# Kernel optimization log

Hardware: AMD Instinct MI355X
Metric: run time of the kernel (lower is better)

The kernel has to match this reference:

```python
import jax, jax.numpy as jnp
import numpy as np

NUM_BITS = 10
MEM_SIZE = 2 ** NUM_BITS  # 1024
HIDDEN = 1024
INPUT = 1024
BATCH = 16384
LN_EPS = 1e-5


def setup_inputs() -> dict:
    key = jax.random.key(0)
    ks = jax.random.split(key, 8)
    s = 0.02
    return {
        "x": jax.random.normal(ks[0], (BATCH, INPUT), jnp.float32),
        "h_prev": jax.random.normal(ks[1], (BATCH, HIDDEN), jnp.float32),
        "memory": jax.random.normal(ks[2], (MEM_SIZE, HIDDEN), jnp.float32),
        "W_w": jax.random.normal(ks[3], (HIDDEN, INPUT), jnp.float32) * s,
        "W_b": jnp.zeros((HIDDEN,), jnp.float32),
        "U_w": jax.random.normal(ks[4], (HIDDEN, HIDDEN), jnp.float32) * s,
        "U_b": jnp.zeros((HIDDEN,), jnp.float32),
        "Q_w": jax.random.normal(ks[5], (HIDDEN, HIDDEN), jnp.float32) * s,
        "Q_b": jnp.zeros((HIDDEN,), jnp.float32),
        "M_w": jax.random.normal(ks[6], (NUM_BITS, HIDDEN), jnp.float32) * s,
        "M_b": jnp.zeros((NUM_BITS,), jnp.float32),
        "ln_g": jnp.ones((HIDDEN,), jnp.float32),
        "ln_b": jnp.zeros((HIDDEN,), jnp.float32),
    }


def reference(x, h_prev, memory, W_w, W_b, U_w, U_b, Q_w, Q_b, M_w, M_b, ln_g, ln_b):
    # Binary address from h_prev (eval-mode hard threshold, non-differentiable)
    powers = jnp.asarray(2 ** np.arange(NUM_BITS - 1, -1, -1), dtype=x.dtype)  # [num_bits]
    logits = h_prev @ M_w.T + M_b                              # [B, num_bits]
    binary = (jax.nn.sigmoid(logits) > 0.5).astype(x.dtype)    # hard bits
    index = jnp.clip((binary * powers).sum(-1).astype(jnp.int32), 0, MEM_SIZE - 1)  # [B]
    h_mem = memory[index]                                      # gather [B, H]
    # Fused linear combine + LayerNorm + sigmoid
    pre = x @ W_w.T + W_b + h_prev @ U_w.T + U_b + h_mem @ Q_w.T + Q_b  # [B, H]
    mu = pre.mean(-1, keepdims=True)
    var = ((pre - mu) ** 2).mean(-1, keepdims=True)            # biased var (torch LN)
    norm = (pre - mu) * jax.lax.rsqrt(var + LN_EPS)
    return jax.nn.sigmoid(norm * ln_g + ln_b)                  # h_new [B, H]
```

## Files before the change

kernel.cpp:

```cpp
#include <hip/hip_runtime.h>

#define BATCH   16384
#define HIDDEN  1024
#define K2      2048
#define MEMSZ   1024
#define NBITS   10

#define BM 256
#define BN 256
#define BK 64
#define NT (K2 / BK)

#define MQB     64
#define U_BM    262144
#define U_TOT   2359296
#define SBLK    2304
#define SSTRIDE (SBLK * 256)
#define BBLK    (BATCH / 8)

typedef __bf16 bf16x8 __attribute__((ext_vector_type(8)));
typedef float  f32x4  __attribute__((ext_vector_type(4)));
typedef unsigned short u16x8 __attribute__((ext_vector_type(8)));

__device__ __forceinline__ unsigned short f2bf(float f) {
    unsigned int u = __float_as_uint(f);
    u += 0x7FFFu + ((u >> 16) & 1u);
    return (unsigned short)(u >> 16);
}

__device__ __forceinline__ u16x8 f2bf8(float4 a, float4 b) {
    u16x8 r;
    r[0] = f2bf(a.x); r[1] = f2bf(a.y); r[2] = f2bf(a.z); r[3] = f2bf(a.w);
    r[4] = f2bf(b.x); r[5] = f2bf(b.y); r[6] = f2bf(b.z); r[7] = f2bf(b.w);
    return r;
}

__device__ __forceinline__ ushort4 f2bf4(float4 a) {
    ushort4 r;
    r.x = f2bf(a.x); r.y = f2bf(a.y); r.z = f2bf(a.z); r.w = f2bf(a.w);
    return r;
}

__device__ __forceinline__ void gload_lds16(const void* g, void* l) {
    __builtin_amdgcn_global_load_lds(
        (const __attribute__((address_space(1))) unsigned int*)g,
        (__attribute__((address_space(3))) unsigned int*)l,
        16, 0, 0);
}

__global__ __launch_bounds__(256) void front_kernel(
        const float* __restrict__ W, const float* __restrict__ U,
        const float* __restrict__ x, const float* __restrict__ h_prev,
        const float* __restrict__ memory, const float* __restrict__ Q,
        const float* __restrict__ M_w, const float* __restrict__ M_b,
        unsigned short* __restrict__ Bm, unsigned short* __restrict__ A,
        float* __restrict__ MQ, int* __restrict__ idxbuf) {
    __shared__ alignas(16) char shmem[40960];

    if (blockIdx.x < MQB) {
        unsigned short* As = reinterpret_cast<unsigned short*>(shmem);
        unsigned short* Bs = reinterpret_cast<unsigned short*>(shmem + 8192);

        const int mb = blockIdx.x >> 3;
        const int nb = blockIdx.x & 7;
        const int t    = threadIdx.x;
        const int lane = t & 63;
        const int w    = t >> 6;
        const int wr   = w >> 1, wc = w & 1;
        const int rr   = lane & 15, rq = lane >> 4;
        const int srow = t >> 1;
        const int scol = (t & 1) * 16;
        const int swr  = (srow & 3) << 4;

        f32x4 acc[4][4] = {};

        for (int kt = 0; kt < 32; ++kt) {
            const int k0 = kt * 32;
            const float* ap = memory + (size_t)(mb * 128 + srow) * 1024 + k0 + scol;
            const float* bp = Q      + (size_t)(nb * 128 + srow) * 1024 + k0 + scol;
            float4 a0 = *reinterpret_cast<const float4*>(ap);
            float4 a1 = *reinterpret_cast<const float4*>(ap + 4);
            float4 a2 = *reinterpret_cast<const float4*>(ap + 8);
            float4 a3 = *reinterpret_cast<const float4*>(ap + 12);
            float4 b0 = *reinterpret_cast<const float4*>(bp);
            float4 b1 = *reinterpret_cast<const float4*>(bp + 4);
            float4 b2 = *reinterpret_cast<const float4*>(bp + 8);
            float4 b3 = *reinterpret_cast<const float4*>(bp + 12);
            __syncthreads();
            {
                char* ar = reinterpret_cast<char*>(As) + srow * 64;
                char* br = reinterpret_cast<char*>(Bs) + srow * 64;
                *reinterpret_cast<u16x8*>(ar + ((scol * 2)      ^ swr)) = f2bf8(a0, a1);
                *reinterpret_cast<u16x8*>(ar + ((scol * 2 + 16) ^ swr)) = f2bf8(a2, a3);
                *reinterpret_cast<u16x8*>(br + ((scol * 2)      ^ swr)) = f2bf8(b0, b1);
                *reinterpret_cast<u16x8*>(br + ((scol * 2 + 16) ^ swr)) = f2bf8(b2, b3);
            }
            __syncthreads();
            bf16x8 af[4], bfv[4];
#pragma unroll
            for (int m = 0; m < 4; ++m) {
                int r = wr * 64 + m * 16 + rr;
                af[m] = *reinterpret_cast<const bf16x8*>(
                    reinterpret_cast<const char*>(As) + r * 64 + ((rq * 16) ^ ((r & 3) << 4)));
            }
#pragma unroll
            for (int n = 0; n < 4; ++n) {
                int r = wc * 64 + n * 16 + rr;
                bfv[n] = *reinterpret_cast<const bf16x8*>(
                    reinterpret_cast<const char*>(Bs) + r * 64 + ((rq * 16) ^ ((r & 3) << 4)));
            }
#pragma unroll
            for (int m = 0; m < 4; ++m)
#pragma unroll
                for (int n = 0; n < 4; ++n)
                    acc[m][n] = __builtin_amdgcn_mfma_f32_16x16x32_bf16(
                        af[m], bfv[n], acc[m][n], 0, 0, 0);
        }

#pragma unroll
        for (int m = 0; m < 4; ++m)
#pragma unroll
            for (int n = 0; n < 4; ++n) {
                int gcol = nb * 128 + wc * 64 + n * 16 + rr;
#pragma unroll
                for (int j = 0; j < 4; ++j) {
                    int grow = mb * 128 + wr * 64 + m * 16 + rq * 4 + j;
                    MQ[(size_t)grow * 1024 + gcol] = acc[m][n][j];
                }
            }
        return;
    }

    if (blockIdx.x < MQB + SBLK) {
        const int u0 = (blockIdx.x - MQB) * 256 + threadIdx.x;
        const float* s4[4];
        unsigned short* d4[4];
#pragma unroll
        for (int i = 0; i < 4; ++i) {
            int u = u0 + i * SSTRIDE;
            if (u < U_BM) {
                int n  = u >> 8;
                int k8 = (u & 255) << 3;
                s4[i] = (k8 < 1024) ? (W + (size_t)n * 1024 + k8)
                                    : (U + (size_t)n * 1024 + (k8 - 1024));
                d4[i] = Bm + (size_t)n * K2 + k8;
            } else {
                int e = (u - U_BM) << 3;
                int row = e >> 10, col = e & 1023;
                s4[i] = x + (size_t)row * HIDDEN + col;
                d4[i] = A + (size_t)row * K2 + col;
            }
        }
        float4 va[4], vb[4];
#pragma unroll
        for (int i = 0; i < 4; ++i) {
            va[i] = *reinterpret_cast<const float4*>(s4[i]);
            vb[i] = *reinterpret_cast<const float4*>(s4[i] + 4);
        }
        __builtin_amdgcn_sched_barrier(0);
#pragma unroll
        for (int i = 0; i < 4; ++i)
            *reinterpret_cast<u16x8*>(d4[i]) = f2bf8(va[i], vb[i]);
        return;
    }

    float* mw = reinterpret_cast<float*>(shmem);
    for (int i = threadIdx.x; i < (NBITS * HIDDEN) / 4; i += 256)
        reinterpret_cast<float4*>(mw)[i] = reinterpret_cast<const float4*>(M_w)[i];
    __syncthreads();

    const int wv   = threadIdx.x >> 6;
    const int lane = threadIdx.x & 63;
    const int row0 = ((blockIdx.x - MQB - SBLK) * 4 + wv) * 2;
    const int c4   = lane * 4;

    float4 h[2][4];
#pragma unroll
    for (int r = 0; r < 2; ++r) {
        const float* hr = h_prev + (size_t)(row0 + r) * HIDDEN;
#pragma unroll
        for (int seg = 0; seg < 4; ++seg)
            h[r][seg] = *reinterpret_cast<const float4*>(hr + seg * 256 + c4);
    }

    float s[2][NBITS];
#pragma unroll
    for (int j = 0; j < NBITS; ++j) {
        const float* mj = mw + j * HIDDEN;
        float4 m[4];
#pragma unroll
        for (int seg = 0; seg < 4; ++seg)
            m[seg] = *reinterpret_cast<const float4*>(mj + seg * 256 + c4);
#pragma unroll
        for (int r = 0; r < 2; ++r) {
            float acc = 0.f;
#pragma unroll
            for (int seg = 0; seg < 4; ++seg)
                acc += h[r][seg].x * m[seg].x + h[r][seg].y * m[seg].y
                     + h[r][seg].z * m[seg].z + h[r][seg].w * m[seg].w;
            s[r][j] = acc;
        }
    }
#pragma unroll
    for (int off = 32; off >= 1; off >>= 1) {
#pragma unroll
        for (int r = 0; r < 2; ++r)
#pragma unroll
            for (int j = 0; j < NBITS; ++j)
                s[r][j] += __shfl_xor(s[r][j], off, 64);
    }
#pragma unroll
    for (int r = 0; r < 2; ++r) {
        int idx = 0;
#pragma unroll
        for (int j = 0; j < NBITS; ++j)
            if (s[r][j] + M_b[j] > 0.f) idx |= 1 << (NBITS - 1 - j);
        if (lane == 0) idxbuf[row0 + r] = idx;
    }

#pragma unroll
    for (int r = 0; r < 2; ++r) {
        unsigned short* arow = A + (size_t)(row0 + r) * K2 + 1024;
#pragma unroll
        for (int seg = 0; seg < 4; ++seg)
            *reinterpret_cast<ushort4*>(arow + seg * 256 + c4) = f2bf4(h[r][seg]);
    }
}


__device__ __forceinline__ void stage_g(const unsigned short* __restrict__ src,
                                        int rowbase, int kt, int g,
                                        unsigned short* ldsTile, int t) {
    const int o      = g * 8192 + t * 16;
    const int row    = o >> 7;
    const int inner  = o & 127;
    const int sinner = inner ^ ((row & 7) << 4);
    const char* gp = reinterpret_cast<const char*>(
                         src + (size_t)(rowbase + row) * K2 + kt * BK) + sinner;
    gload_lds16(gp, reinterpret_cast<char*>(ldsTile) + o);
}

__device__ __forceinline__ bf16x8 ldsfrag(const unsigned short* tile, int row,
                                          int kbyte_x_sw) {
    return *reinterpret_cast<const bf16x8*>(
        reinterpret_cast<const char*>(tile) + row * 128 + kbyte_x_sw);
}

#define PH_BAR()                                                     \
    do {                                                             \
        asm volatile("" ::: "memory");                               \
        __builtin_amdgcn_s_barrier();                                \
        asm volatile("" ::: "memory");                               \
    } while (0)

#define LGKM(N)                                                      \
    do {                                                             \
        asm volatile("s_waitcnt lgkmcnt(" #N ")" ::: "memory");      \
        __builtin_amdgcn_sched_barrier(0);                           \
    } while (0)

#define MFMA_Q(AF, BF, MB, NB)                                                 \
    {                                                                          \
        __builtin_amdgcn_s_setprio(1);                                         \
        _Pragma("unroll") for (int m_ = 0; m_ < 4; ++m_)                       \
        _Pragma("unroll") for (int n_ = 0; n_ < 2; ++n_)                       \
        _Pragma("unroll") for (int kk_ = 0; kk_ < 2; ++kk_)                    \
            acc[(MB) + m_][(NB) + n_] =                                        \
                __builtin_amdgcn_mfma_f32_16x16x32_bf16(                       \
                    AF[m_][kk_], BF[n_][kk_],                                  \
                    acc[(MB) + m_][(NB) + n_], 0, 0, 0);                       \
        __builtin_amdgcn_s_setprio(0);                                         \
    }

__global__ __launch_bounds__(512, 2) void gemm_kernel(
        const unsigned short* __restrict__ A,
        const unsigned short* __restrict__ Bm,
        float* __restrict__ C) {
    __shared__ alignas(16) unsigned short lds[2][2][BM * BK];

    const int bid  = blockIdx.x;
    const int wgid = (bid & 7) * 32 + (bid >> 3);
    const int mblk = wgid >> 2;
    const int nblk = wgid & 3;

    const int t    = threadIdx.x;
    const int lane = t & 63;
    const int w    = t >> 6;
    const int wr   = w >> 2;
    const int wc   = w & 3;
    const int rr   = lane & 15;
    const int rq   = lane >> 4;
    const int sw   = (rr & 7) << 4;
    const int rqb  = rq * 16;
    const int wrb  = wr * 128;
    const int wcb  = wc * 64;

    const int arow = mblk * BM;
    const int brow = nblk * BN;

    f32x4 acc[8][4] = {};

    {
#pragma unroll
        for (int g = 0; g < 4; ++g) stage_g(A,  arow, 0, g, &lds[0][0][0], t);
#pragma unroll
        for (int g = 0; g < 4; ++g) stage_g(Bm, brow, 0, g, &lds[0][1][0], t);
#pragma unroll
        for (int g = 0; g < 4; ++g) stage_g(Bm, brow, 1, g, &lds[1][1][0], t);
#pragma unroll
        for (int g = 0; g < 4; ++g) stage_g(A,  arow, 1, g, &lds[1][0][0], t);
        asm volatile("s_waitcnt vmcnt(8)" ::: "memory");
        asm volatile("" ::: "memory");
        __builtin_amdgcn_s_barrier();
    }

    bf16x8 af  [4][2];
    bf16x8 af2 [4][2];
    bf16x8 bfr01[2][2];
    bf16x8 bfr23[2][2];

#pragma unroll
    for (int m = 0; m < 4; ++m) {
        af[m][0] = ldsfrag(&lds[0][0][0], wrb + m * 16 + rr, (rqb) ^ sw);
        af[m][1] = ldsfrag(&lds[0][0][0], wrb + m * 16 + rr, (64 + rqb) ^ sw);
    }
#pragma unroll
    for (int n = 0; n < 2; ++n) {
        bfr01[n][0] = ldsfrag(&lds[0][1][0], wcb + n * 16 + rr, (rqb) ^ sw);
        bfr01[n][1] = ldsfrag(&lds[0][1][0], wcb + n * 16 + rr, (64 + rqb) ^ sw);
    }

    for (int kt = 0; kt < NT; ++kt) {
        const int c = kt & 1;
        const unsigned short* At  = &lds[c][0][0];
        const unsigned short* Bt  = &lds[c][1][0];
        const unsigned short* nxA = &lds[c ^ 1][0][0];
        const unsigned short* nxB = &lds[c ^ 1][1][0];
        unsigned short* curA = &lds[c][0][0];
        unsigned short* curB = &lds[c][1][0];
        const bool pf1 = (kt + 1 < NT);
        const bool pf2 = (kt + 2 < NT);

        PH_BAR();
#pragma unroll
        for (int n = 0; n < 2; ++n) {
            bfr23[n][0] = ldsfrag(Bt, wcb + 32 + n * 16 + rr, (rqb) ^ sw);
            bfr23[n][1] = ldsfrag(Bt, wcb + 32 + n * 16 + rr, (64 + rqb) ^ sw);
        }
        af2[0][0] = ldsfrag(At, wrb + 64 + rr, (rqb) ^ sw);
        af2[0][1] = ldsfrag(At, wrb + 64 + rr, (64 + rqb) ^ sw);
        LGKM(6);
        MFMA_Q(af, bfr01, 0, 0);

        PH_BAR();
#pragma unroll
        for (int m = 1; m < 4; ++m) {
            af2[m][0] = ldsfrag(At, wrb + 64 + m * 16 + rr, (rqb) ^ sw);
            af2[m][1] = ldsfrag(At, wrb + 64 + m * 16 + rr, (64 + rqb) ^ sw);
        }
        LGKM(8);
        MFMA_Q(af, bfr23, 0, 2);
        __builtin_amdgcn_sched_barrier(0);
        asm volatile("s_waitcnt vmcnt(0)" ::: "memory");
        asm volatile("" ::: "memory");

        PH_BAR();
        if (pf2) {
            stage_g(Bm, brow, kt + 2, 0, curB, t);
            stage_g(Bm, brow, kt + 2, 1, curB, t);
            stage_g(Bm, brow, kt + 2, 2, curB, t);
            stage_g(Bm, brow, kt + 2, 3, curB, t);
        }
        if (pf1) {
#pragma unroll
            for (int m = 0; m < 3; ++m) {
                af[m][0] = ldsfrag(nxA, wrb + m * 16 + rr, (rqb) ^ sw);
                af[m][1] = ldsfrag(nxA, wrb + m * 16 + rr, (64 + rqb) ^ sw);
            }
            LGKM(6);
        } else {
            LGKM(0);
        }
        MFMA_Q(af2, bfr01, 4, 0);

        PH_BAR();
        if (pf2) {
            stage_g(A, arow, kt + 2, 0, curA, t);
            stage_g(A, arow, kt + 2, 1, curA, t);
            stage_g(A, arow, kt + 2, 2, curA, t);
            stage_g(A, arow, kt + 2, 3, curA, t);
        }
        if (pf1) {
            af[3][0] = ldsfrag(nxA, wrb + 48 + rr, (rqb) ^ sw);
            af[3][1] = ldsfrag(nxA, wrb + 48 + rr, (64 + rqb) ^ sw);
#pragma unroll
            for (int n = 0; n < 2; ++n) {
                bfr01[n][0] = ldsfrag(nxB, wcb + n * 16 + rr, (rqb) ^ sw);
                bfr01[n][1] = ldsfrag(nxB, wcb + n * 16 + rr, (64 + rqb) ^ sw);
            }
        }
        MFMA_Q(af2, bfr23, 4, 2);
    }

#pragma unroll
    for (int mi = 0; mi < 8; ++mi) {
#pragma unroll
        for (int n = 0; n < 4; ++n) {
            const int gcol = nblk * BN + wcb + n * 16 + rr;
#pragma unroll
            for (int j = 0; j < 4; ++j) {
                const int grow = mblk * BM + wrb + mi * 16 + rq * 4 + j;
                C[(size_t)grow * HIDDEN + gcol] = acc[mi][n][j];
            }
        }
    }
}

__global__ __launch_bounds__(256) void ln_kernel(
        float* __restrict__ C,
        const int* __restrict__ idxbuf,
        const float* __restrict__ MQ,
        const float* __restrict__ W_b, const float* __restrict__ U_b,
        const float* __restrict__ Q_b, const float* __restrict__ ln_g,
        const float* __restrict__ ln_b) {
    const int row = blockIdx.x;
    const int t   = threadIdx.x;
    const int midx = idxbuf[row];
    float4* rowp = reinterpret_cast<float4*>(C + (size_t)row * HIDDEN);
    const float4* mqp = reinterpret_cast<const float4*>(MQ + (size_t)midx * HIDDEN);

    float4 p  = rowp[t];
    float4 mq = mqp[t];
    float4 bw = reinterpret_cast<const float4*>(W_b)[t];
    float4 bu = reinterpret_cast<const float4*>(U_b)[t];
    float4 bq = reinterpret_cast<const float4*>(Q_b)[t];
    p.x += mq.x + bw.x + bu.x + bq.x;
    p.y += mq.y + bw.y + bu.y + bq.y;
    p.z += mq.z + bw.z + bu.z + bq.z;
    p.w += mq.w + bw.w + bu.w + bq.w;

    float s  = p.x + p.y + p.z + p.w;
    float sq = p.x * p.x + p.y * p.y + p.z * p.z + p.w * p.w;
#pragma unroll
    for (int off = 32; off >= 1; off >>= 1) {
        s  += __shfl_xor(s,  off, 64);
        sq += __shfl_xor(sq, off, 64);
    }
    __shared__ float red[8];
    const int lane = t & 63, w = t >> 6;
    if (lane == 0) { red[w] = s; red[4 + w] = sq; }
    __syncthreads();
    const float S    = red[0] + red[1] + red[2] + red[3];
    const float SQ   = red[4] + red[5] + red[6] + red[7];
    const float mean = S * (1.0f / HIDDEN);
    const float var  = SQ * (1.0f / HIDDEN) - mean * mean;
    const float rstd = rsqrtf(var + 1e-5f);

    float4 g = reinterpret_cast<const float4*>(ln_g)[t];
    float4 b = reinterpret_cast<const float4*>(ln_b)[t];
    float4 o;
    o.x = 1.f / (1.f + __expf(-((p.x - mean) * rstd * g.x + b.x)));
    o.y = 1.f / (1.f + __expf(-((p.y - mean) * rstd * g.y + b.y)));
    o.z = 1.f / (1.f + __expf(-((p.z - mean) * rstd * g.z + b.z)));
    o.w = 1.f / (1.f + __expf(-((p.w - mean) * rstd * g.w + b.w)));
    rowp[t] = o;
}

extern "C" void kernel_launch(void* const* d_in, const int* in_sizes, int n_in,
                              void* d_out, int out_size, void* d_ws, size_t ws_size,
                              hipStream_t stream) {
    const float* x      = (const float*)d_in[0];
    const float* h_prev = (const float*)d_in[1];
    const float* memory = (const float*)d_in[2];
    const float* W_w    = (const float*)d_in[3];
    const float* W_b    = (const float*)d_in[4];
    const float* U_w    = (const float*)d_in[5];
    const float* U_b    = (const float*)d_in[6];
    const float* Q_w    = (const float*)d_in[7];
    const float* Q_b    = (const float*)d_in[8];
    const float* M_w    = (const float*)d_in[9];
    const float* M_b    = (const float*)d_in[10];
    const float* ln_g   = (const float*)d_in[11];
    const float* ln_b   = (const float*)d_in[12];

    char* ws = (char*)d_ws;
    unsigned short* A   = (unsigned short*)(ws);
    unsigned short* Bm  = (unsigned short*)(ws + 67108864);
    float*          MQ  = (float*)         (ws + 71303168);
    int*            idx = (int*)           (ws + 75497472);

    float* pre = (float*)d_out;

    hipLaunchKernelGGL(front_kernel, dim3(MQB + SBLK + BBLK), dim3(256), 0, stream,
                       W_w, U_w, x, h_prev, memory, Q_w, M_w, M_b,
                       Bm, A, MQ, idx);
    hipLaunchKernelGGL(gemm_kernel, dim3((BATCH / BM) * (HIDDEN / BN)), dim3(512), 0, stream,
                       A, Bm, pre);
    hipLaunchKernelGGL(ln_kernel, dim3(BATCH), dim3(256), 0, stream,
                       pre, idx, MQ, W_b, U_b, Q_b, ln_g, ln_b);
}
```

Before: 164.2 us.

## Split memory·Q GEMM into separate kernel and drop LDS from front kernel

```diff
diff --git a/kernel.cpp b/kernel.cpp
--- a/kernel.cpp
+++ b/kernel.cpp
@@ -11,12 +11,11 @@
 #define BK 64
 #define NT (K2 / BK)
 
-#define MQB     64
+#define BBLK    2048
 #define U_BM    262144
 #define U_TOT   2359296
 #define SBLK    2304
 #define SSTRIDE (SBLK * 256)
-#define BBLK    (BATCH / 8)
 
 typedef __bf16 bf16x8 __attribute__((ext_vector_type(8)));
 typedef float  f32x4  __attribute__((ext_vector_type(4)));
@@ -51,180 +50,174 @@
 __global__ __launch_bounds__(256) void front_kernel(
         const float* __restrict__ W, const float* __restrict__ U,
         const float* __restrict__ x, const float* __restrict__ h_prev,
-        const float* __restrict__ memory, const float* __restrict__ Q,
         const float* __restrict__ M_w, const float* __restrict__ M_b,
         unsigned short* __restrict__ Bm, unsigned short* __restrict__ A,
-        float* __restrict__ MQ, int* __restrict__ idxbuf) {
-    __shared__ alignas(16) char shmem[40960];
-
-    if (blockIdx.x < MQB) {
-        unsigned short* As = reinterpret_cast<unsigned short*>(shmem);
-        unsigned short* Bs = reinterpret_cast<unsigned short*>(shmem + 8192);
-
-        const int mb = blockIdx.x >> 3;
-        const int nb = blockIdx.x & 7;
-        const int t    = threadIdx.x;
-        const int lane = t & 63;
-        const int w    = t >> 6;
-        const int wr   = w >> 1, wc = w & 1;
-        const int rr   = lane & 15, rq = lane >> 4;
-        const int srow = t >> 1;
-        const int scol = (t & 1) * 16;
-        const int swr  = (srow & 3) << 4;
-
-        f32x4 acc[4][4] = {};
-
-        for (int kt = 0; kt < 32; ++kt) {
-            const int k0 = kt * 32;
-            const float* ap = memory + (size_t)(mb * 128 + srow) * 1024 + k0 + scol;
-            const float* bp = Q      + (size_t)(nb * 128 + srow) * 1024 + k0 + scol;
-            float4 a0 = *reinterpret_cast<const float4*>(ap);
-            float4 a1 = *reinterpret_cast<const float4*>(ap + 4);
-            float4 a2 = *reinterpret_cast<const float4*>(ap + 8);
-            float4 a3 = *reinterpret_cast<const float4*>(ap + 12);
-            float4 b0 = *reinterpret_cast<const float4*>(bp);
-            float4 b1 = *reinterpret_cast<const float4*>(bp + 4);
-            float4 b2 = *reinterpret_cast<const float4*>(bp + 8);
-            float4 b3 = *reinterpret_cast<const float4*>(bp + 12);
-            __syncthreads();
-            {
-                char* ar = reinterpret_cast<char*>(As) + srow * 64;
-                char* br = reinterpret_cast<char*>(Bs) + srow * 64;
-                *reinterpret_cast<u16x8*>(ar + ((scol * 2)      ^ swr)) = f2bf8(a0, a1);
-                *reinterpret_cast<u16x8*>(ar + ((scol * 2 + 16) ^ swr)) = f2bf8(a2, a3);
-                *reinterpret_cast<u16x8*>(br + ((scol * 2)      ^ swr)) = f2bf8(b0, b1);
-                *reinterpret_cast<u16x8*>(br + ((scol * 2 + 16) ^ swr)) = f2bf8(b2, b3);
+        int* __restrict__ idxbuf) {
+    if (blockIdx.x < BBLK) {
+        const int wv   = threadIdx.x >> 6;
+        const int lane = threadIdx.x & 63;
+        const int row0 = (blockIdx.x * 4 + wv) * 2;
+        const int c4   = lane * 4;
+
+        float4 h[2][4];
+#pragma unroll
+        for (int r = 0; r < 2; ++r) {
+            const float* hr = h_prev + (size_t)(row0 + r) * HIDDEN;
+#pragma unroll
+            for (int seg = 0; seg < 4; ++seg)
+                h[r][seg] = *reinterpret_cast<const float4*>(hr + seg * 256 + c4);
+        }
+
+        float s[2][NBITS];
+#pragma unroll
+        for (int j = 0; j < NBITS; ++j) {
+            const float* mj = M_w + (size_t)j * HIDDEN;
+            float4 m[4];
+#pragma unroll
+            for (int seg = 0; seg < 4; ++seg)
+                m[seg] = *reinterpret_cast<const float4*>(mj + seg * 256 + c4);
+#pragma unroll
+            for (int r = 0; r < 2; ++r) {
+                float acc = 0.f;
+#pragma unroll
+                for (int seg = 0; seg < 4; ++seg)
+                    acc += h[r][seg].x * m[seg].x + h[r][seg].y * m[seg].y
+                         + h[r][seg].z * m[seg].z + h[r][seg].w * m[seg].w;
+                s[r][j] = acc;
             }
-            __syncthreads();
-            bf16x8 af[4], bfv[4];
-#pragma unroll
-            for (int m = 0; m < 4; ++m) {
-                int r = wr * 64 + m * 16 + rr;
-                af[m] = *reinterpret_cast<const bf16x8*>(
-                    reinterpret_cast<const char*>(As) + r * 64 + ((rq * 16) ^ ((r & 3) << 4)));
+        }
+#pragma unroll
+        for (int off = 32; off >= 1; off >>= 1) {
+#pragma unroll
+            for (int r = 0; r < 2; ++r)
+#pragma unroll
+                for (int j = 0; j < NBITS; ++j)
+                    s[r][j] += __shfl_xor(s[r][j], off, 64);
+        }
+#pragma unroll
+        for (int r = 0; r < 2; ++r) {
+            int idx = 0;
+#pragma unroll
+            for (int j = 0; j < NBITS; ++j)
+                if (s[r][j] + M_b[j] > 0.f) idx |= 1 << (NBITS - 1 - j);
+            if (lane == 0) idxbuf[row0 + r] = idx;
+        }
+
+#pragma unroll
+        for (int r = 0; r < 2; ++r) {
+            unsigned short* arow = A + (size_t)(row0 + r) * K2 + 1024;
+#pragma unroll
+            for (int seg = 0; seg < 4; ++seg)
+                *reinterpret_cast<ushort4*>(arow + seg * 256 + c4) = f2bf4(h[r][seg]);
+        }
+        return;
+    }
+
+    const int u0 = (blockIdx.x - BBLK) * 256 + threadIdx.x;
+    const float* s4[4];
+    unsigned short* d4[4];
+#pragma unroll
+    for (int i = 0; i < 4; ++i) {
+        int u = u0 + i * SSTRIDE;
+        if (u < U_BM) {
+            int n  = u >> 8;
+            int k8 = (u & 255) << 3;
+            s4[i] = (k8 < 1024) ? (W + (size_t)n * 1024 + k8)
+                                : (U + (size_t)n * 1024 + (k8 - 1024));
+            d4[i] = Bm + (size_t)n * K2 + k8;
+        } else {
+            int e = (u - U_BM) << 3;
+            int row = e >> 10, col = e & 1023;
+            s4[i] = x + (size_t)row * HIDDEN + col;
+            d4[i] = A + (size_t)row * K2 + col;
+        }
+    }
+    float4 va[4], vb[4];
+#pragma unroll
+    for (int i = 0; i < 4; ++i) {
+        va[i] = *reinterpret_cast<const float4*>(s4[i]);
+        vb[i] = *reinterpret_cast<const float4*>(s4[i] + 4);
+    }
+    __builtin_amdgcn_sched_barrier(0);
+#pragma unroll
+    for (int i = 0; i < 4; ++i)
+        *reinterpret_cast<u16x8*>(d4[i]) = f2bf8(va[i], vb[i]);
+}
+
+__global__ __launch_bounds__(256) void mq_kernel(
+        const float* __restrict__ memory,
+        const float* __restrict__ Q,
+        float* __restrict__ MQ) {
+    __shared__ unsigned short As[128 * 32];
+    __shared__ unsigned short Bs[128 * 32];
+
+    const int mb = blockIdx.x >> 3;
+    const int nb = blockIdx.x & 7;
+    const int t    = threadIdx.x;
+    const int lane = t & 63;
+    const int w    = t >> 6;
+    const int wr   = w >> 1, wc = w & 1;
+    const int rr   = lane & 15, rq = lane >> 4;
+    const int srow = t >> 1;
+    const int scol = (t & 1) * 16;
+    const int swr  = (srow & 3) << 4;
+
+    f32x4 acc[4][4] = {};
+
+    for (int kt = 0; kt < 32; ++kt) {
+        const int k0 = kt * 32;
+        const float* ap = memory + (size_t)(mb * 128 + srow) * 1024 + k0 + scol;
+        const float* bp = Q      + (size_t)(nb * 128 + srow) * 1024 + k0 + scol;
+        float4 a0 = *reinterpret_cast<const float4*>(ap);
+        float4 a1 = *reinterpret_cast<const float4*>(ap + 4);
+        float4 a2 = *reinterpret_cast<const float4*>(ap + 8);
+        float4 a3 = *reinterpret_cast<const float4*>(ap + 12);
+        float4 b0 = *reinterpret_cast<const float4*>(bp);
+        float4 b1 = *reinterpret_cast<const float4*>(bp + 4);
+        float4 b2 = *reinterpret_cast<const float4*>(bp + 8);
+        float4 b3 = *reinterpret_cast<const float4*>(bp + 12);
+        __syncthreads();
+        {
+            char* ar = reinterpret_cast<char*>(As) + srow * 64;
+            char* br = reinterpret_cast<char*>(Bs) + srow * 64;
+            *reinterpret_cast<u16x8*>(ar + ((scol * 2)      ^ swr)) = f2bf8(a0, a1);
+            *reinterpret_cast<u16x8*>(ar + ((scol * 2 + 16) ^ swr)) = f2bf8(a2, a3);
+            *reinterpret_cast<u16x8*>(br + ((scol * 2)      ^ swr)) = f2bf8(b0, b1);
+            *reinterpret_cast<u16x8*>(br + ((scol * 2 + 16) ^ swr)) = f2bf8(b2, b3);
+        }
+        __syncthreads();
+        bf16x8 af[4], bfv[4];
+#pragma unroll
+        for (int m = 0; m < 4; ++m) {
+            int r = wr * 64 + m * 16 + rr;
+            af[m] = *reinterpret_cast<const bf16x8*>(
+                reinterpret_cast<const char*>(As) + r * 64 + ((rq * 16) ^ ((r & 3) << 4)));
+        }
+#pragma unroll
+        for (int n = 0; n < 4; ++n) {
+            int r = wc * 64 + n * 16 + rr;
+            bfv[n] = *reinterpret_cast<const bf16x8*>(
+                reinterpret_cast<const char*>(Bs) + r * 64 + ((rq * 16) ^ ((r & 3) << 4)));
+        }
+#pragma unroll
+        for (int m = 0; m < 4; ++m)
+#pragma unroll
+            for (int n = 0; n < 4; ++n)
+                acc[m][n] = __builtin_amdgcn_mfma_f32_16x16x32_bf16(
+                    af[m], bfv[n], acc[m][n], 0, 0, 0);
+    }
+
+#pragma unroll
+    for (int m = 0; m < 4; ++m)
+#pragma unroll
+        for (int n = 0; n < 4; ++n) {
+            int gcol = nb * 128 + wc * 64 + n * 16 + rr;
+#pragma unroll
+            for (int j = 0; j < 4; ++j) {
+                int grow = mb * 128 + wr * 64 + m * 16 + rq * 4 + j;
+                MQ[(size_t)grow * 1024 + gcol] = acc[m][n][j];
             }
-#pragma unroll
-            for (int n = 0; n < 4; ++n) {
-                int r = wc * 64 + n * 16 + rr;
-                bfv[n] = *reinterpret_cast<const bf16x8*>(
-                    reinterpret_cast<const char*>(Bs) + r * 64 + ((rq * 16) ^ ((r & 3) << 4)));
-            }
-#pragma unroll
-            for (int m = 0; m < 4; ++m)
-#pragma unroll
-                for (int n = 0; n < 4; ++n)
-                    acc[m][n] = __builtin_amdgcn_mfma_f32_16x16x32_bf16(
-                        af[m], bfv[n], acc[m][n], 0, 0, 0);
-        }
-
-#pragma unroll
-        for (int m = 0; m < 4; ++m)
-#pragma unroll
-            for (int n = 0; n < 4; ++n) {
-                int gcol = nb * 128 + wc * 64 + n * 16 + rr;
-#pragma unroll
-                for (int j = 0; j < 4; ++j) {
-                    int grow = mb * 128 + wr * 64 + m * 16 + rq * 4 + j;
-                    MQ[(size_t)grow * 1024 + gcol] = acc[m][n][j];
-                }
-            }
-        return;
-    }
-
-    if (blockIdx.x < MQB + SBLK) {
-        const int u0 = (blockIdx.x - MQB) * 256 + threadIdx.x;
-        const float* s4[4];
-        unsigned short* d4[4];
-#pragma unroll
-        for (int i = 0; i < 4; ++i) {
-            int u = u0 + i * SSTRIDE;
-            if (u < U_BM) {
-                int n  = u >> 8;
-                int k8 = (u & 255) << 3;
-                s4[i] = (k8 < 1024) ? (W + (size_t)n * 1024 + k8)
-                                    : (U + (size_t)n * 1024 + (k8 - 1024));
-                d4[i] = Bm + (size_t)n * K2 + k8;
-            } else {
-                int e = (u - U_BM) << 3;
-                int row = e >> 10, col = e & 1023;
-                s4[i] = x + (size_t)row * HIDDEN + col;
-                d4[i] = A + (size_t)row * K2 + col;
-            }
-        }
-        float4 va[4], vb[4];
-#pragma unroll
-        for (int i = 0; i < 4; ++i) {
-            va[i] = *reinterpret_cast<const float4*>(s4[i]);
-            vb[i] = *reinterpret_cast<const float4*>(s4[i] + 4);
-        }
-        __builtin_amdgcn_sched_barrier(0);
-#pragma unroll
-        for (int i = 0; i < 4; ++i)
-            *reinterpret_cast<u16x8*>(d4[i]) = f2bf8(va[i], vb[i]);
-        return;
-    }
-
-    float* mw = reinterpret_cast<float*>(shmem);
-    for (int i = threadIdx.x; i < (NBITS * HIDDEN) / 4; i += 256)
-        reinterpret_cast<float4*>(mw)[i] = reinterpret_cast<const float4*>(M_w)[i];
-    __syncthreads();
-
-    const int wv   = threadIdx.x >> 6;
-    const int lane = threadIdx.x & 63;
-    const int row0 = ((blockIdx.x - MQB - SBLK) * 4 + wv) * 2;
-    const int c4   = lane * 4;
-
-    float4 h[2][4];
-#pragma unroll
-    for (int r = 0; r < 2; ++r) {
-        const float* hr = h_prev + (size_t)(row0 + r) * HIDDEN;
-#pragma unroll
-        for (int seg = 0; seg < 4; ++seg)
-            h[r][seg] = *reinterpret_cast<const float4*>(hr + seg * 256 + c4);
-    }
-
-    float s[2][NBITS];
-#pragma unroll
-    for (int j = 0; j < NBITS; ++j) {
-        const float* mj = mw + j * HIDDEN;
-        float4 m[4];
-#pragma unroll
-        for (int seg = 0; seg < 4; ++seg)
-            m[seg] = *reinterpret_cast<const float4*>(mj + seg * 256 + c4);
-#pragma unroll
-        for (int r = 0; r < 2; ++r) {
-            float acc = 0.f;
-#pragma unroll
-            for (int seg = 0; seg < 4; ++seg)
-                acc += h[r][seg].x * m[seg].x + h[r][seg].y * m[seg].y
-                     + h[r][seg].z * m[seg].z + h[r][seg].w * m[seg].w;
-            s[r][j] = acc;
-        }
-    }
-#pragma unroll
-    for (int off = 32; off >= 1; off >>= 1) {
-#pragma unroll
-        for (int r = 0; r < 2; ++r)
-#pragma unroll
-            for (int j = 0; j < NBITS; ++j)
-                s[r][j] += __shfl_xor(s[r][j], off, 64);
-    }
-#pragma unroll
-    for (int r = 0; r < 2; ++r) {
-        int idx = 0;
-#pragma unroll
-        for (int j = 0; j < NBITS; ++j)
-            if (s[r][j] + M_b[j] > 0.f) idx |= 1 << (NBITS - 1 - j);
-        if (lane == 0) idxbuf[row0 + r] = idx;
-    }
-
-#pragma unroll
-    for (int r = 0; r < 2; ++r) {
-        unsigned short* arow = A + (size_t)(row0 + r) * K2 + 1024;
-#pragma unroll
-        for (int seg = 0; seg < 4; ++seg)
-            *reinterpret_cast<ushort4*>(arow + seg * 256 + c4) = f2bf4(h[r][seg]);
-    }
+        }
 }
 
 
@@ -491,9 +484,10 @@
 
     float* pre = (float*)d_out;
 
-    hipLaunchKernelGGL(front_kernel, dim3(MQB + SBLK + BBLK), dim3(256), 0, stream,
-                       W_w, U_w, x, h_prev, memory, Q_w, M_w, M_b,
-                       Bm, A, MQ, idx);
+    hipLaunchKernelGGL(front_kernel, dim3(BBLK + SBLK), dim3(256), 0, stream,
+                       W_w, U_w, x, h_prev, M_w, M_b, Bm, A, idx);
+    hipLaunchKernelGGL(mq_kernel, dim3(64), dim3(256), 0, stream,
+                       memory, Q_w, MQ);
     hipLaunchKernelGGL(gemm_kernel, dim3((BATCH / BM) * (HIDDEN / BN)), dim3(512), 0, stream,
                        A, Bm, pre);
     hipLaunchKernelGGL(ln_kernel, dim3(BATCH), dim3(256), 0, stream,
```

Result: slower. 181.5 us (+10.6%).
